# Optimization experiments

Measured on AMD Instinct MI355X. Metric: run time of the kernel, lower is better.

The kernel has to match this reference:

```python
import jax, jax.numpy as jnp
import numpy as np

B = 2          # graphs (images)
GRID = 13      # patches per spatial dim -> N = 169 patches per image
N = GRID * GRID
NN = B * N     # total nodes
C = 256        # hidden_dim / out_channels per head
H = 4          # attention heads
L = 3          # GAT layers
LRELU_SLOPE = 0.2
LN_EPS = 1e-5


def _dense_edges():
    # fully-connected directed graph (i != j) per image, as in create_graph
    idx = np.arange(N)
    src, dst = np.meshgrid(idx, idx, indexing='ij')
    mask = src != dst
    src, dst = src[mask], dst[mask]              # [N*(N-1)]
    offs = (np.arange(B) * N)[:, None]
    e_src = (src[None, :] + offs).reshape(-1)
    e_dst = (dst[None, :] + offs).reshape(-1)
    return e_src.astype(np.int32), e_dst.astype(np.int32)


def setup_inputs() -> dict:
    key = jax.random.key(0)
    ks = jax.random.split(key, 8)
    s = 0.05
    e_src, e_dst = _dense_edges()
    return {
        'x':   jax.random.normal(ks[0], (NN, C), jnp.float32),
        'Wl':  jax.random.normal(ks[1], (L, C, H * C), jnp.float32) * s,
        'bl':  jnp.zeros((L, H * C), jnp.float32),
        'Wr':  jax.random.normal(ks[2], (L, C, H * C), jnp.float32) * s,
        'br':  jnp.zeros((L, H * C), jnp.float32),
        'att': jax.random.normal(ks[3], (L, H, C), jnp.float32) * s,
        'bias': jnp.zeros((L, C), jnp.float32),
        'ln_g': jnp.ones((L, C), jnp.float32),
        'ln_b': jnp.zeros((L, C), jnp.float32),
        'W1':  jax.random.normal(ks[4], (L, C, 2 * C), jnp.float32) * s,
        'b1':  jnp.zeros((L, 2 * C), jnp.float32),
        'W2':  jax.random.normal(ks[5], (L, 2 * C, C), jnp.float32) * s,
        'b2':  jnp.zeros((L, C), jnp.float32),
        'edge_src': jnp.asarray(e_src),
        'edge_dst': jnp.asarray(e_dst),
        'batch_ids': jnp.repeat(jnp.arange(B, dtype=jnp.int32), N),
    }


def _gatv2(x, Wl, bl, Wr, br, att, bias, src, dst, n_nodes):
    # PyG GATv2Conv, concat=False (mean over heads)
    xl = (x @ Wl + bl).reshape(n_nodes, H, C)   # source transform
    xr = (x @ Wr + br).reshape(n_nodes, H, C)   # target transform
    e = jax.nn.leaky_relu(xl[src] + xr[dst], LRELU_SLOPE)     # [E,H,C]
    logits = jnp.einsum('ehc,hc->eh', e, att)                 # [E,H]
    m = jax.ops.segment_max(logits, dst, num_segments=n_nodes)
    a = jnp.exp(logits - m[dst])
    z = jax.ops.segment_sum(a, dst, num_segments=n_nodes)
    alpha = a / (z[dst] + 1e-16)                              # softmax per target
    msg = alpha[:, :, None] * xl[src]                         # [E,H,C]
    agg = jax.ops.segment_sum(msg, dst, num_segments=n_nodes) # [N,H,C]
    return agg.mean(axis=1) + bias


def _layernorm(x, g, b):
    mu = x.mean(-1, keepdims=True)
    var = jnp.mean((x - mu) ** 2, -1, keepdims=True)
    return (x - mu) * jax.lax.rsqrt(var + LN_EPS) * g + b


def reference(x, Wl, bl, Wr, br, att, bias, ln_g, ln_b, W1, b1, W2, b2,
              edge_src, edge_dst, batch_ids):
    n_nodes = x.shape[0]
    for l in range(L):
        residual = x
        h = _gatv2(x, Wl[l], bl[l], Wr[l], br[l], att[l], bias[l],
                   edge_src, edge_dst, n_nodes)
        h = _layernorm(h, ln_g[l], ln_b[l])
        mlp = jnp.maximum(h @ W1[l] + b1[l], 0.0) @ W2[l] + b2[l]
        x = residual + mlp
    # global mean pool per graph
    sums = jax.ops.segment_sum(x, batch_ids, num_segments=B)
    cnts = jax.ops.segment_sum(jnp.ones((n_nodes, 1), x.dtype), batch_ids,
                               num_segments=B)
    return sums / cnts
```

## Files before the change

kernel.cpp:

```cpp
#include <hip/hip_runtime.h>
#include <hip/hip_bf16.h>

typedef __hip_bfloat16 bf16;
typedef __attribute__((ext_vector_type(4))) float f32x4;
typedef __attribute__((ext_vector_type(8))) unsigned short u16x8;
typedef __attribute__((ext_vector_type(4))) unsigned short u16x4;
typedef __bf16 bf16x8 __attribute__((ext_vector_type(8)));

#define NNODES 169
#define NNTOT  338
#define CH     256
#define NH     4
#define NL     3
#define SPAD   176
#define LN_EPS 1e-5f

__device__ __forceinline__ float b2f(bf16 v) { return __bfloat162float(v); }
__device__ __forceinline__ float lrelu(float v) { return fmaxf(v, 0.2f * v); }
__device__ __forceinline__ float ldm(const void* p, size_t i, int isbf) {
    return isbf ? b2f(((const bf16*)p)[i]) : ((const float*)p)[i];
}
__device__ __forceinline__ int sniff_bf(const void* lng) {
    return ((((const unsigned*)lng)[0] & 0xFFFFu) == 0x3F80u) ? 1 : 0;
}
__device__ __forceinline__ unsigned short f2bf_rn(float f) {
    unsigned u = __float_as_uint(f);
    u += 0x7FFFu + ((u >> 16) & 1u);
    return (unsigned short)(u >> 16);
}
__device__ __forceinline__ float bfb2f(unsigned short h) {
    return __uint_as_float(((unsigned)h) << 16);
}

__global__ __launch_bounds__(256) void k_wprep(
    const void* __restrict__ Wl, const void* __restrict__ Wr,
    const void* __restrict__ W1, const void* __restrict__ W2,
    unsigned short* __restrict__ wlT, unsigned short* __restrict__ wrT,
    unsigned short* __restrict__ w1T, unsigned short* __restrict__ w2T,
    const void* __restrict__ lng)
{
    __shared__ unsigned short sH[64 * 72];
    __shared__ unsigned short sL[64 * 72];
    const int isbf = sniff_bf(lng);
    int t = blockIdx.x;
    const void* src; unsigned short* dst; int K, N;
    if (t < 384)      { K = 256; N = 1024; src = (t < 192) ? Wl : Wr;
                        dst = (t < 192) ? wlT : wrT; t = t % 192; }
    else if (t < 480) { K = 256; N = 512;  src = W1; dst = w1T; t -= 384; }
    else              { K = 512; N = 256;  src = W2; dst = w2T; t -= 480; }
    const int ntiles = N / 64;
    const int tpl = (K / 64) * ntiles;
    const int l = t / tpl; t %= tpl;
    const int k0 = (t / ntiles) * 64, n0 = (t % ntiles) * 64;
    const size_t loPlane = (size_t)NL * K * N;
    const int tid = threadIdx.x;

    const int kk = tid >> 2, q = tid & 3;
    if (isbf) {
        const bf16* srow = (const bf16*)src + ((size_t)l * K + k0 + kk) * N + n0;
        #pragma unroll
        for (int i = 0; i < 4; i++) {
            const int c = q * 4 + i * 16;
            const int2 w = *(const int2*)(srow + c);
            const unsigned short u0 = (unsigned short)(w.x & 0xFFFF);
            const unsigned short u1 = (unsigned short)(((unsigned)w.x) >> 16);
            const unsigned short u2 = (unsigned short)(w.y & 0xFFFF);
            const unsigned short u3 = (unsigned short)(((unsigned)w.y) >> 16);
            sH[kk * 72 + c + 0] = u0; sL[kk * 72 + c + 0] = 0;
            sH[kk * 72 + c + 1] = u1; sL[kk * 72 + c + 1] = 0;
            sH[kk * 72 + c + 2] = u2; sL[kk * 72 + c + 2] = 0;
            sH[kk * 72 + c + 3] = u3; sL[kk * 72 + c + 3] = 0;
        }
    } else {
        const float* srow = (const float*)src + ((size_t)l * K + k0 + kk) * N + n0;
        #pragma unroll
        for (int i = 0; i < 4; i++) {
            const int c = q * 4 + i * 16;
            const float4 v4 = *(const float4*)(srow + c);
            const float vv[4] = { v4.x, v4.y, v4.z, v4.w };
            #pragma unroll
            for (int j = 0; j < 4; j++) {
                const unsigned short h = f2bf_rn(vv[j]);
                sH[kk * 72 + c + j] = h;
                sL[kk * 72 + c + j] = f2bf_rn(vv[j] - bfb2f(h));
            }
        }
    }
    __syncthreads();
    for (int u = tid; u < 512; u += 256) {
        const int n = u >> 3, k8 = (u & 7) * 8;
        u16x8 hh, ll;
        #pragma unroll
        for (int j = 0; j < 8; j++) {
            hh[j] = sH[(k8 + j) * 72 + n];
            ll[j] = sL[(k8 + j) * 72 + n];
        }
        unsigned short* dh = dst + ((size_t)l * N + n0 + n) * K + k0 + k8;
        *(u16x8*)dh = hh;
        *(u16x8*)(dh + loPlane) = ll;
    }
}

__global__ __launch_bounds__(256) void k_gemm_mfma(
    const void* __restrict__ A, int a_raw, int K, int N,
    const unsigned short* __restrict__ wH0, const unsigned short* __restrict__ wL0,
    const unsigned short* __restrict__ wH1, const unsigned short* __restrict__ wL1,
    const void* __restrict__ bias0, const void* __restrict__ bias1, size_t oB,
    const void* __restrict__ res, int r_raw,
    float* __restrict__ out0, float* __restrict__ out1,
    float* __restrict__ xlT, int mode, const void* __restrict__ lng)
{
    __shared__ unsigned short sAh[32 * 40], sAl[32 * 40];
    __shared__ unsigned short sBh[64 * 40], sBl[64 * 40];
    const int isbf = sniff_bf(lng);
    const int z = blockIdx.z;
    const unsigned short* wH = z ? wH1 : wH0;
    const unsigned short* wL = z ? wL1 : wL0;
    const void* bias = z ? bias1 : bias0;
    float* out = z ? out1 : out0;
    const int a_bf = a_raw ? isbf : 0;
    const int tid = threadIdx.x;
    const int wave = tid >> 6, lane = tid & 63, l15 = lane & 15, g = lane >> 4;
    const int m0 = blockIdx.x * 32, n0 = blockIdx.y * 64;

    const int ar = tid >> 3, ak = (tid & 7) * 4;
    const int bn = tid >> 2, boct = tid & 3;

    f32x4 acc0 = {0.f, 0.f, 0.f, 0.f};
    f32x4 acc1 = {0.f, 0.f, 0.f, 0.f};
    const float* Af = (const float*)A;

    for (int k0 = 0; k0 < K; k0 += 32) {
        unsigned short h4[4] = {0, 0, 0, 0}, l4[4] = {0, 0, 0, 0};
        {
            const int grow = m0 + ar;
            if (grow < NNTOT) {
                const size_t ai = (size_t)grow * K + k0 + ak;
                if (a_bf) {
                    const int2 w = *(const int2*)((const bf16*)A + ai);
                    h4[0] = (unsigned short)(w.x & 0xFFFF);
                    h4[1] = (unsigned short)(((unsigned)w.x) >> 16);
                    h4[2] = (unsigned short)(w.y & 0xFFFF);
                    h4[3] = (unsigned short)(((unsigned)w.y) >> 16);
                } else {
                    const float4 t = *(const float4*)(Af + ai);
                    const float vv[4] = { t.x, t.y, t.z, t.w };
                    #pragma unroll
                    for (int j = 0; j < 4; j++) {
                        h4[j] = f2bf_rn(vv[j]);
                        l4[j] = f2bf_rn(vv[j] - bfb2f(h4[j]));
                    }
                }
            }
        }
        const size_t bi = (size_t)(n0 + bn) * K + k0 + boct * 8;
        const u16x8 bhv = *(const u16x8*)(wH + bi);
        const u16x8 blv = *(const u16x8*)(wL + bi);
        __syncthreads();
        {
            u16x4 ha, la;
            ha[0] = h4[0]; ha[1] = h4[1]; ha[2] = h4[2]; ha[3] = h4[3];
            la[0] = l4[0]; la[1] = l4[1]; la[2] = l4[2]; la[3] = l4[3];
            *(u16x4*)&sAh[ar * 40 + ak] = ha;
            *(u16x4*)&sAl[ar * 40 + ak] = la;
            *(u16x8*)&sBh[bn * 40 + boct * 8] = bhv;
            *(u16x8*)&sBl[bn * 40 + boct * 8] = blv;
        }
        __syncthreads();
        const bf16x8 a_h0 = *(const bf16x8*)&sAh[l15 * 40 + g * 8];
        const bf16x8 a_h1 = *(const bf16x8*)&sAh[(16 + l15) * 40 + g * 8];
        const bf16x8 a_l0 = *(const bf16x8*)&sAl[l15 * 40 + g * 8];
        const bf16x8 a_l1 = *(const bf16x8*)&sAl[(16 + l15) * 40 + g * 8];
        const bf16x8 b_h  = *(const bf16x8*)&sBh[(wave * 16 + l15) * 40 + g * 8];
        const bf16x8 b_l  = *(const bf16x8*)&sBl[(wave * 16 + l15) * 40 + g * 8];
        acc0 = __builtin_amdgcn_mfma_f32_16x16x32_bf16(a_h0, b_h, acc0, 0, 0, 0);
        acc1 = __builtin_amdgcn_mfma_f32_16x16x32_bf16(a_h1, b_h, acc1, 0, 0, 0);
        acc0 = __builtin_amdgcn_mfma_f32_16x16x32_bf16(a_l0, b_h, acc0, 0, 0, 0);
        acc1 = __builtin_amdgcn_mfma_f32_16x16x32_bf16(a_l1, b_h, acc1, 0, 0, 0);
        acc0 = __builtin_amdgcn_mfma_f32_16x16x32_bf16(a_h0, b_l, acc0, 0, 0, 0);
        acc1 = __builtin_amdgcn_mfma_f32_16x16x32_bf16(a_h1, b_l, acc1, 0, 0, 0);
    }

    const int col = n0 + wave * 16 + l15;
    const float bv = ldm(bias, oB + col, isbf);
    #pragma unroll
    for (int mi = 0; mi < 2; mi++) {
        const f32x4 a = mi ? acc1 : acc0;
        #pragma unroll
        for (int r = 0; r < 4; r++) {
            const int row = m0 + mi * 16 + g * 4 + r;
            if (row >= NNTOT) continue;
            float v = a[r] + bv;
            if (mode == 1) v = fmaxf(v, 0.f);
            if (mode == 2) v += ldm(res, (size_t)row * N + col, r_raw ? isbf : 0);
            out[(size_t)row * N + col] = v;
            if (mode == 0 && z == 0) {
                const int hh = col >> 8, cc = col & 255;
                const int gg = (row >= NNODES) ? 1 : 0;
                const int ss = row - gg * NNODES;
                xlT[((size_t)(gg * NH + hh) * CH + cc) * SPAD + ss] = v;
            }
        }
    }
}

__global__ __launch_bounds__(192) void k_logits_sm(
    const float* __restrict__ xlT, const float* __restrict__ xr,
    const void* __restrict__ att, size_t oA,
    float* __restrict__ alphaR, const void* __restrict__ lng)
{
    __shared__ float s_att[CH];
    __shared__ float s_xr[2 * CH];
    __shared__ float s_tile[32 * SPAD];
    __shared__ float s_log[2 * SPAD];
    const int isbf = sniff_bf(lng);
    const int g = blockIdx.z, h = blockIdx.y, d0 = blockIdx.x * 2;
    const int tid = threadIdx.x, lane = tid & 63, wv = tid >> 6;

    for (int idx = tid; idx < CH; idx += 192)
        s_att[idx] = ldm(att, oA + h * CH + idx, isbf);
    for (int idx = tid; idx < 2 * CH; idx += 192) {
        const int i = idx >> 8, c = idx & 255, d = d0 + i;
        s_xr[idx] = (d < NNODES)
            ? xr[(size_t)(g * NNODES + d) * (NH * CH) + h * CH + c] : 0.f;
    }

    float l0 = 0.f, l1 = 0.f;
    const int s = tid;
    const float4* src = (const float4*)(xlT + ((size_t)(g * NH + h) * CH) * SPAD);
    for (int ch = 0; ch < 8; ch++) {
        __syncthreads();
        #pragma unroll 2
        for (int i = tid; i < 32 * SPAD / 4; i += 192)
            ((float4*)s_tile)[i] = src[ch * (32 * SPAD / 4) + i];
        __syncthreads();
        if (s < NNODES) {
            const int cb = ch * 32;
            #pragma unroll
            for (int c = 0; c < 32; c++) {
                const float v = s_tile[c * SPAD + s];
                const float a = s_att[cb + c];
                l0 += a * lrelu(v + s_xr[cb + c]);
                l1 += a * lrelu(v + s_xr[CH + cb + c]);
            }
        }
    }
    if (s < NNODES) { s_log[s] = l0; s_log[SPAD + s] = l1; }
    __syncthreads();

    if (wv < 2) {
        const int d = d0 + wv;
        const float* row = s_log + wv * SPAD;
        const int s0 = lane, s1 = lane + 64, s2 = lane + 128;
        const float v0 = (s0 < NNODES && s0 != d) ? row[s0] : -1e30f;
        const float v1 = (s1 < NNODES && s1 != d) ? row[s1] : -1e30f;
        const float v2 = (s2 < NNODES && s2 != d) ? row[s2] : -1e30f;
        float mx = fmaxf(v0, fmaxf(v1, v2));
        mx = fmaxf(mx, __shfl_xor(mx, 32)); mx = fmaxf(mx, __shfl_xor(mx, 16));
        mx = fmaxf(mx, __shfl_xor(mx, 8));  mx = fmaxf(mx, __shfl_xor(mx, 4));
        mx = fmaxf(mx, __shfl_xor(mx, 2));  mx = fmaxf(mx, __shfl_xor(mx, 1));
        const float e0 = expf(v0 - mx), e1 = expf(v1 - mx), e2 = expf(v2 - mx);
        float zz = e0 + e1 + e2;
        zz += __shfl_xor(zz, 32); zz += __shfl_xor(zz, 16); zz += __shfl_xor(zz, 8);
        zz += __shfl_xor(zz, 4);  zz += __shfl_xor(zz, 2);  zz += __shfl_xor(zz, 1);
        const float sc = 0.25f / (zz + 1e-16f);
        if (d < NNODES) {
            float* arow = alphaR + ((size_t)(g * NH + h) * NNODES + d) * SPAD;
            if (s0 < NNODES) arow[s0] = e0 * sc;
            if (s1 < NNODES) arow[s1] = e1 * sc;
            if (s2 < NNODES) arow[s2] = e2 * sc;
        }
    }
}

__global__ __launch_bounds__(256) void k_agg(
    const float* __restrict__ alphaR, const float* __restrict__ xl,
    float* __restrict__ part)
{
    __shared__ float s_a[32 * 33];
    __shared__ float s_x[32 * 64];
    const int gh = blockIdx.z, g = gh >> 2, h = gh & 3;
    const int d0 = blockIdx.x * 32, c0 = blockIdx.y * 64;
    const int tid = threadIdx.x;
    const int dr = (tid >> 4) * 2, cq = (tid & 15) * 4;
    const int sr = tid >> 3, sc4 = (tid & 7) * 4;
    const int xc8 = (tid & 7) * 8;

    float acc[2][4] = {{0.f,0.f,0.f,0.f},{0.f,0.f,0.f,0.f}};

    for (int s0 = 0; s0 < NNODES; s0 += 32) {
        __syncthreads();
        {
            const int d = d0 + sr;
            const float* ap = alphaR + ((size_t)gh * NNODES + d) * SPAD + s0 + sc4;
            const int ok = (d < NNODES);
            s_a[sr * 33 + sc4 + 0] = (ok && s0 + sc4 + 0 < NNODES) ? ap[0] : 0.f;
            s_a[sr * 33 + sc4 + 1] = (ok && s0 + sc4 + 1 < NNODES) ? ap[1] : 0.f;
            s_a[sr * 33 + sc4 + 2] = (ok && s0 + sc4 + 2 < NNODES) ? ap[2] : 0.f;
            s_a[sr * 33 + sc4 + 3] = (ok && s0 + sc4 + 3 < NNODES) ? ap[3] : 0.f;
        }
        {
            const int sg = s0 + sr;
            if (sg < NNODES) {
                const float* xp = xl + (size_t)(g * NNODES + sg) * (NH * CH) + h * CH + c0 + xc8;
                *(float4*)&s_x[sr * 64 + xc8]     = *(const float4*)(xp);
                *(float4*)&s_x[sr * 64 + xc8 + 4] = *(const float4*)(xp + 4);
            } else {
                #pragma unroll
                for (int j = 0; j < 8; j++) s_x[sr * 64 + xc8 + j] = 0.f;
            }
        }
        __syncthreads();
        #pragma unroll
        for (int k = 0; k < 32; k++) {
            const float a0 = s_a[(dr + 0) * 33 + k];
            const float a1 = s_a[(dr + 1) * 33 + k];
            const float4 xv = *(const float4*)&s_x[k * 64 + cq];
            acc[0][0] += a0 * xv.x; acc[0][1] += a0 * xv.y;
            acc[0][2] += a0 * xv.z; acc[0][3] += a0 * xv.w;
            acc[1][0] += a1 * xv.x; acc[1][1] += a1 * xv.y;
            acc[1][2] += a1 * xv.z; acc[1][3] += a1 * xv.w;
        }
    }
    #pragma unroll
    for (int i = 0; i < 2; i++) {
        const int d = d0 + dr + i;
        if (d >= NNODES) continue;
        float4 v;
        v.x = acc[i][0]; v.y = acc[i][1]; v.z = acc[i][2]; v.w = acc[i][3];
        *(float4*)(part + ((size_t)h * NNTOT + g * NNODES + d) * CH + c0 + cq) = v;
    }
}

__global__ __launch_bounds__(256) void k_ln(
    const float* __restrict__ part,
    const void* __restrict__ bias, size_t oB,
    const void* __restrict__ ln_g, size_t oG,
    const void* __restrict__ ln_b, size_t oBt,
    float* __restrict__ h_out, const void* __restrict__ lng)
{
    __shared__ float s_red[8];
    const int isbf = sniff_bf(lng);
    const int node = blockIdx.x, c = threadIdx.x;
    const int lane = c & 63, wv = c >> 6;

    float vch = part[((size_t)0 * NNTOT + node) * CH + c]
              + part[((size_t)1 * NNTOT + node) * CH + c]
              + part[((size_t)2 * NNTOT + node) * CH + c]
              + part[((size_t)3 * NNTOT + node) * CH + c]
              + ldm(bias, oB + c, isbf);

    float s1 = vch, s2 = vch * vch;
    s1 += __shfl_xor(s1, 32); s2 += __shfl_xor(s2, 32);
    s1 += __shfl_xor(s1, 16); s2 += __shfl_xor(s2, 16);
    s1 += __shfl_xor(s1, 8);  s2 += __shfl_xor(s2, 8);
    s1 += __shfl_xor(s1, 4);  s2 += __shfl_xor(s2, 4);
    s1 += __shfl_xor(s1, 2);  s2 += __shfl_xor(s2, 2);
    s1 += __shfl_xor(s1, 1);  s2 += __shfl_xor(s2, 1);
    if (lane == 0) { s_red[wv] = s1; s_red[4 + wv] = s2; }
    __syncthreads();
    const float S1 = s_red[0] + s_red[1] + s_red[2] + s_red[3];
    const float S2 = s_red[4] + s_red[5] + s_red[6] + s_red[7];
    const float mu  = S1 * (1.f / CH);
    const float var = S2 * (1.f / CH) - mu * mu;
    const float o = (vch - mu) * rsqrtf(var + LN_EPS) * ldm(ln_g, oG + c, isbf)
                  + ldm(ln_b, oBt + c, isbf);
    h_out[(size_t)node * CH + c] = o;
}

__global__ __launch_bounds__(256) void k_pool(const float* __restrict__ x,
                                              void* __restrict__ out,
                                              const void* __restrict__ lng) {
    const int isbf = sniff_bf(lng);
    const int g = blockIdx.x, c = threadIdx.x;
    float s = 0.f;
    const float* p = x + (size_t)g * NNODES * CH + c;
    for (int n = 0; n < NNODES; n++) s += p[(size_t)n * CH];
    const float v = s * (1.f / NNODES);
    if (isbf) ((bf16*)out)[g * CH + c] = __float2bfloat16(v);
    else      ((float*)out)[g * CH + c] = v;
}

extern "C" void kernel_launch(void* const* d_in, const int* in_sizes, int n_in,
                              void* d_out, int out_size, void* d_ws, size_t ws_size,
                              hipStream_t stream)
{
    const void* x_in = d_in[0];
    const void* Wl   = d_in[1];
    const void* bl   = d_in[2];
    const void* Wr   = d_in[3];
    const void* br   = d_in[4];
    const void* att  = d_in[5];
    const void* bias = d_in[6];
    const void* lng  = d_in[7];
    const void* lnb  = d_in[8];
    const void* W1   = d_in[9];
    const void* b1   = d_in[10];
    const void* W2   = d_in[11];
    const void* b2   = d_in[12];

    float* ws     = (float*)d_ws;
    float* xl     = ws;
    float* xr     = xl + (size_t)NNTOT * NH * CH;
    float* xlT    = xr + (size_t)NNTOT * NH * CH;
    float* alphaR = xlT + (size_t)2 * NH * CH * SPAD;
    float* part   = alphaR + (size_t)2 * NH * NNODES * SPAD;
    float* h_ln   = part + (size_t)NH * NNTOT * CH;
    float* m1     = h_ln + (size_t)NNTOT * CH;
    float* xa     = m1 + (size_t)NNTOT * 2 * CH;
    float* xb     = xa + (size_t)NNTOT * CH;

    unsigned short* wbt = (unsigned short*)(xb + (size_t)NNTOT * CH);
    const size_t pLR = (size_t)NL * (NH * CH) * CH;
    const size_t pM  = (size_t)NL * (2 * CH) * CH;
    unsigned short* wlT = wbt;
    unsigned short* wrT = wlT + 2 * pLR;
    unsigned short* w1T = wrT + 2 * pLR;
    unsigned short* w2T = w1T + 2 * pM;
    const size_t lyLR = (size_t)(NH * CH) * CH;
    const size_t lyM  = (size_t)(2 * CH) * CH;

    const size_t sB  = NH * CH;
    const size_t sC  = CH;
    const size_t sB1 = 2 * CH;

    const void* x_l[3] = { x_in, xa, xb };
    float*      x_o[3] = { xa, xb, xa };

    k_wprep<<<dim3(576), 256, 0, stream>>>(Wl, Wr, W1, W2, wlT, wrT, w1T, w2T, lng);

    for (int l = 0; l < NL; l++) {
        const int israw = (l == 0);
        k_gemm_mfma<<<dim3(11, 16, 2), 256, 0, stream>>>(
            x_l[l], israw, CH, NH * CH,
            wlT + l * lyLR, wlT + pLR + l * lyLR,
            wrT + l * lyLR, wrT + pLR + l * lyLR,
            bl, br, (size_t)l * sB,
            nullptr, 0,
            xl, xr, xlT, 0, lng);
        k_logits_sm<<<dim3(85, NH, 2), 192, 0, stream>>>(
            xlT, xr, att, (size_t)l * sB, alphaR, lng);
        k_agg<<<dim3(6, 4, 8), 256, 0, stream>>>(alphaR, xl, part);
        k_ln<<<dim3(NNTOT), 256, 0, stream>>>(
            part, bias, (size_t)l * sC, lng, (size_t)l * sC, lnb, (size_t)l * sC,
            h_ln, lng);
        k_gemm_mfma<<<dim3(11, 8, 1), 256, 0, stream>>>(
            h_ln, 0, CH, 2 * CH,
            w1T + l * lyM, w1T + pM + l * lyM,
            w1T + l * lyM, w1T + pM + l * lyM,
            b1, b1, (size_t)l * sB1,
            nullptr, 0,
            m1, m1, nullptr, 1, lng);
        k_gemm_mfma<<<dim3(11, 4, 1), 256, 0, stream>>>(
            m1, 0, 2 * CH, CH,
            w2T + l * lyM, w2T + pM + l * lyM,
            w2T + l * lyM, w2T + pM + l * lyM,
            b2, b2, (size_t)l * sC,
            x_l[l], israw,
            x_o[l], x_o[l], nullptr, 2, lng);
    }

    k_pool<<<dim3(2), 256, 0, stream>>>(xa, d_out, lng);
}
```

Before: 327.7 us.

## Fuse attention softmax with aggregation and LayerNorm with first MLP GEMM

Merges the logits/softmax kernel with the alpha-weighted aggregation so alpha stays in shared memory and is never written to global memory. Each block now handles four targets instead of two, and the per-channel aggregation reads xl directly from global memory. It also fuses LayerNorm into the first MLP GEMM, normalising rows into split-bf16 shared tiles before the MFMA loop. This removes two kernel launches per layer and the h_ln and alphaR round trips. The trade-offs are that the aggregation now runs as scalar FMAs with strided global loads instead of a tiled kernel, and each LN block recomputes normalisation across all N tiles.

Measured after the change: 328.0 us. No clear change (+0.1%).

```diff
diff --git a/kernel.cpp b/kernel.cpp
--- a/kernel.cpp
+++ b/kernel.cpp
@@ -62,14 +62,12 @@
         for (int i = 0; i < 4; i++) {
             const int c = q * 4 + i * 16;
             const int2 w = *(const int2*)(srow + c);
-            const unsigned short u0 = (unsigned short)(w.x & 0xFFFF);
-            const unsigned short u1 = (unsigned short)(((unsigned)w.x) >> 16);
-            const unsigned short u2 = (unsigned short)(w.y & 0xFFFF);
-            const unsigned short u3 = (unsigned short)(((unsigned)w.y) >> 16);
-            sH[kk * 72 + c + 0] = u0; sL[kk * 72 + c + 0] = 0;
-            sH[kk * 72 + c + 1] = u1; sL[kk * 72 + c + 1] = 0;
-            sH[kk * 72 + c + 2] = u2; sL[kk * 72 + c + 2] = 0;
-            sH[kk * 72 + c + 3] = u3; sL[kk * 72 + c + 3] = 0;
+            sH[kk * 72 + c + 0] = (unsigned short)(w.x & 0xFFFF);
+            sH[kk * 72 + c + 1] = (unsigned short)(((unsigned)w.x) >> 16);
+            sH[kk * 72 + c + 2] = (unsigned short)(w.y & 0xFFFF);
+            sH[kk * 72 + c + 3] = (unsigned short)(((unsigned)w.y) >> 16);
+            sL[kk * 72 + c + 0] = 0; sL[kk * 72 + c + 1] = 0;
+            sL[kk * 72 + c + 2] = 0; sL[kk * 72 + c + 3] = 0;
         }
     } else {
         const float* srow = (const float*)src + ((size_t)l * K + k0 + kk) * N + n0;
@@ -191,7 +189,6 @@
             const int row = m0 + mi * 16 + g * 4 + r;
             if (row >= NNTOT) continue;
             float v = a[r] + bv;
-            if (mode == 1) v = fmaxf(v, 0.f);
             if (mode == 2) v += ldm(res, (size_t)row * N + col, r_raw ? isbf : 0);
             out[(size_t)row * N + col] = v;
             if (mode == 0 && z == 0) {
@@ -204,34 +201,33 @@
     }
 }
 
-__global__ __launch_bounds__(192) void k_logits_sm(
+__global__ __launch_bounds__(256) void k_attn(
     const float* __restrict__ xlT, const float* __restrict__ xr,
+    const float* __restrict__ xl,
     const void* __restrict__ att, size_t oA,
-    float* __restrict__ alphaR, const void* __restrict__ lng)
+    float* __restrict__ part, const void* __restrict__ lng)
 {
     __shared__ float s_att[CH];
-    __shared__ float s_xr[2 * CH];
+    __shared__ float s_xr[4 * CH];
     __shared__ float s_tile[32 * SPAD];
-    __shared__ float s_log[2 * SPAD];
+    __shared__ float s_log[4 * SPAD];
     const int isbf = sniff_bf(lng);
-    const int g = blockIdx.z, h = blockIdx.y, d0 = blockIdx.x * 2;
+    const int g = blockIdx.z, h = blockIdx.y, d0 = blockIdx.x * 4;
     const int tid = threadIdx.x, lane = tid & 63, wv = tid >> 6;
 
-    for (int idx = tid; idx < CH; idx += 192)
-        s_att[idx] = ldm(att, oA + h * CH + idx, isbf);
-    for (int idx = tid; idx < 2 * CH; idx += 192) {
+    s_att[tid] = ldm(att, oA + h * CH + tid, isbf);
+    for (int idx = tid; idx < 4 * CH; idx += 256) {
         const int i = idx >> 8, c = idx & 255, d = d0 + i;
         s_xr[idx] = (d < NNODES)
             ? xr[(size_t)(g * NNODES + d) * (NH * CH) + h * CH + c] : 0.f;
     }
 
-    float l0 = 0.f, l1 = 0.f;
+    float l0 = 0.f, l1 = 0.f, l2 = 0.f, l3 = 0.f;
     const int s = tid;
     const float4* src = (const float4*)(xlT + ((size_t)(g * NH + h) * CH) * SPAD);
     for (int ch = 0; ch < 8; ch++) {
         __syncthreads();
-        #pragma unroll 2
-        for (int i = tid; i < 32 * SPAD / 4; i += 192)
+        for (int i = tid; i < 32 * SPAD / 4; i += 256)
             ((float4*)s_tile)[i] = src[ch * (32 * SPAD / 4) + i];
         __syncthreads();
         if (s < NNODES) {
@@ -242,15 +238,19 @@
                 const float a = s_att[cb + c];
                 l0 += a * lrelu(v + s_xr[cb + c]);
                 l1 += a * lrelu(v + s_xr[CH + cb + c]);
+                l2 += a * lrelu(v + s_xr[2 * CH + cb + c]);
+                l3 += a * lrelu(v + s_xr[3 * CH + cb + c]);
             }
         }
     }
-    if (s < NNODES) { s_log[s] = l0; s_log[SPAD + s] = l1; }
+    if (s < NNODES) {
+        s_log[s] = l0; s_log[SPAD + s] = l1;
+        s_log[2 * SPAD + s] = l2; s_log[3 * SPAD + s] = l3;
+    }
     __syncthreads();
-
-    if (wv < 2) {
+    {
         const int d = d0 + wv;
-        const float* row = s_log + wv * SPAD;
+        float* row = s_log + wv * SPAD;
         const int s0 = lane, s1 = lane + 64, s2 = lane + 128;
         const float v0 = (s0 < NNODES && s0 != d) ? row[s0] : -1e30f;
         const float v1 = (s1 < NNODES && s1 != d) ? row[s1] : -1e30f;
@@ -264,108 +264,140 @@
         zz += __shfl_xor(zz, 32); zz += __shfl_xor(zz, 16); zz += __shfl_xor(zz, 8);
         zz += __shfl_xor(zz, 4);  zz += __shfl_xor(zz, 2);  zz += __shfl_xor(zz, 1);
         const float sc = 0.25f / (zz + 1e-16f);
-        if (d < NNODES) {
-            float* arow = alphaR + ((size_t)(g * NH + h) * NNODES + d) * SPAD;
-            if (s0 < NNODES) arow[s0] = e0 * sc;
-            if (s1 < NNODES) arow[s1] = e1 * sc;
-            if (s2 < NNODES) arow[s2] = e2 * sc;
-        }
-    }
-}
-
-__global__ __launch_bounds__(256) void k_agg(
-    const float* __restrict__ alphaR, const float* __restrict__ xl,
-    float* __restrict__ part)
-{
-    __shared__ float s_a[32 * 33];
-    __shared__ float s_x[32 * 64];
-    const int gh = blockIdx.z, g = gh >> 2, h = gh & 3;
-    const int d0 = blockIdx.x * 32, c0 = blockIdx.y * 64;
-    const int tid = threadIdx.x;
-    const int dr = (tid >> 4) * 2, cq = (tid & 15) * 4;
-    const int sr = tid >> 3, sc4 = (tid & 7) * 4;
-    const int xc8 = (tid & 7) * 8;
-
-    float acc[2][4] = {{0.f,0.f,0.f,0.f},{0.f,0.f,0.f,0.f}};
-
-    for (int s0 = 0; s0 < NNODES; s0 += 32) {
-        __syncthreads();
-        {
-            const int d = d0 + sr;
-            const float* ap = alphaR + ((size_t)gh * NNODES + d) * SPAD + s0 + sc4;
-            const int ok = (d < NNODES);
-            s_a[sr * 33 + sc4 + 0] = (ok && s0 + sc4 + 0 < NNODES) ? ap[0] : 0.f;
-            s_a[sr * 33 + sc4 + 1] = (ok && s0 + sc4 + 1 < NNODES) ? ap[1] : 0.f;
-            s_a[sr * 33 + sc4 + 2] = (ok && s0 + sc4 + 2 < NNODES) ? ap[2] : 0.f;
-            s_a[sr * 33 + sc4 + 3] = (ok && s0 + sc4 + 3 < NNODES) ? ap[3] : 0.f;
-        }
-        {
-            const int sg = s0 + sr;
-            if (sg < NNODES) {
-                const float* xp = xl + (size_t)(g * NNODES + sg) * (NH * CH) + h * CH + c0 + xc8;
-                *(float4*)&s_x[sr * 64 + xc8]     = *(const float4*)(xp);
-                *(float4*)&s_x[sr * 64 + xc8 + 4] = *(const float4*)(xp + 4);
-            } else {
-                #pragma unroll
-                for (int j = 0; j < 8; j++) s_x[sr * 64 + xc8 + j] = 0.f;
-            }
-        }
-        __syncthreads();
-        #pragma unroll
-        for (int k = 0; k < 32; k++) {
-            const float a0 = s_a[(dr + 0) * 33 + k];
-            const float a1 = s_a[(dr + 1) * 33 + k];
-            const float4 xv = *(const float4*)&s_x[k * 64 + cq];
-            acc[0][0] += a0 * xv.x; acc[0][1] += a0 * xv.y;
-            acc[0][2] += a0 * xv.z; acc[0][3] += a0 * xv.w;
-            acc[1][0] += a1 * xv.x; acc[1][1] += a1 * xv.y;
-            acc[1][2] += a1 * xv.z; acc[1][3] += a1 * xv.w;
-        }
-    }
+        row[s0] = (s0 < NNODES) ? e0 * sc : 0.f;
+        row[s1] = (s1 < NNODES) ? e1 * sc : 0.f;
+        if (s2 < SPAD) row[s2] = (s2 < NNODES) ? e2 * sc : 0.f;
+    }
+    __syncthreads();
+
+    const int c = tid;
+    float a0 = 0.f, a1 = 0.f, a2 = 0.f, a3 = 0.f;
+    const float* xbase = xl + (size_t)g * NNODES * (NH * CH) + h * CH + c;
+    for (int s4 = 0; s4 < 168; s4 += 4) {
+        const float4 q0 = *(const float4*)&s_log[s4];
+        const float4 q1 = *(const float4*)&s_log[SPAD + s4];
+        const float4 q2 = *(const float4*)&s_log[2 * SPAD + s4];
+        const float4 q3 = *(const float4*)&s_log[3 * SPAD + s4];
+        const float x0 = xbase[(size_t)(s4 + 0) * (NH * CH)];
+        const float x1 = xbase[(size_t)(s4 + 1) * (NH * CH)];
+        const float x2 = xbase[(size_t)(s4 + 2) * (NH * CH)];
+        const float x3 = xbase[(size_t)(s4 + 3) * (NH * CH)];
+        a0 += q0.x * x0 + q0.y * x1 + q0.z * x2 + q0.w * x3;
+        a1 += q1.x * x0 + q1.y * x1 + q1.z * x2 + q1.w * x3;
+        a2 += q2.x * x0 + q2.y * x1 + q2.z * x2 + q2.w * x3;
+        a3 += q3.x * x0 + q3.y * x1 + q3.z * x2 + q3.w * x3;
+    }
+    {
+        const float x0 = xbase[(size_t)168 * (NH * CH)];
+        a0 += s_log[168] * x0;            a1 += s_log[SPAD + 168] * x0;
+        a2 += s_log[2 * SPAD + 168] * x0; a3 += s_log[3 * SPAD + 168] * x0;
+    }
+    const float av[4] = { a0, a1, a2, a3 };
     #pragma unroll
-    for (int i = 0; i < 2; i++) {
-        const int d = d0 + dr + i;
-        if (d >= NNODES) continue;
-        float4 v;
-        v.x = acc[i][0]; v.y = acc[i][1]; v.z = acc[i][2]; v.w = acc[i][3];
-        *(float4*)(part + ((size_t)h * NNTOT + g * NNODES + d) * CH + c0 + cq) = v;
-    }
-}
-
-__global__ __launch_bounds__(256) void k_ln(
+    for (int i = 0; i < 4; i++) {
+        const int d = d0 + i;
+        if (d < NNODES)
+            part[((size_t)h * NNTOT + g * NNODES + d) * CH + c] = av[i];
+    }
+}
+
+__global__ __launch_bounds__(256) void k_lnmlp1(
     const float* __restrict__ part,
     const void* __restrict__ bias, size_t oB,
     const void* __restrict__ ln_g, size_t oG,
     const void* __restrict__ ln_b, size_t oBt,
-    float* __restrict__ h_out, const void* __restrict__ lng)
+    const unsigned short* __restrict__ wH, const unsigned short* __restrict__ wL,
+    const void* __restrict__ b1, size_t oB1,
+    float* __restrict__ m1, const void* __restrict__ lng)
 {
-    __shared__ float s_red[8];
+    __shared__ unsigned short sAh[32 * 264], sAl[32 * 264];
+    __shared__ unsigned short sBh[64 * 40], sBl[64 * 40];
+    __shared__ float sPar[3 * CH];
     const int isbf = sniff_bf(lng);
-    const int node = blockIdx.x, c = threadIdx.x;
-    const int lane = c & 63, wv = c >> 6;
-
-    float vch = part[((size_t)0 * NNTOT + node) * CH + c]
-              + part[((size_t)1 * NNTOT + node) * CH + c]
-              + part[((size_t)2 * NNTOT + node) * CH + c]
-              + part[((size_t)3 * NNTOT + node) * CH + c]
-              + ldm(bias, oB + c, isbf);
-
-    float s1 = vch, s2 = vch * vch;
-    s1 += __shfl_xor(s1, 32); s2 += __shfl_xor(s2, 32);
-    s1 += __shfl_xor(s1, 16); s2 += __shfl_xor(s2, 16);
-    s1 += __shfl_xor(s1, 8);  s2 += __shfl_xor(s2, 8);
-    s1 += __shfl_xor(s1, 4);  s2 += __shfl_xor(s2, 4);
-    s1 += __shfl_xor(s1, 2);  s2 += __shfl_xor(s2, 2);
-    s1 += __shfl_xor(s1, 1);  s2 += __shfl_xor(s2, 1);
-    if (lane == 0) { s_red[wv] = s1; s_red[4 + wv] = s2; }
+    const int tid = threadIdx.x;
+    const int wave = tid >> 6, lane = tid & 63, l15 = lane & 15, g = lane >> 4;
+    const int m0 = blockIdx.x * 32, n0 = blockIdx.y * 64;
+
+    sPar[tid]          = ldm(bias, oB + tid, isbf);
+    sPar[CH + tid]     = ldm(ln_g, oG + tid, isbf);
+    sPar[2 * CH + tid] = ldm(ln_b, oBt + tid, isbf);
     __syncthreads();
-    const float S1 = s_red[0] + s_red[1] + s_red[2] + s_red[3];
-    const float S2 = s_red[4] + s_red[5] + s_red[6] + s_red[7];
-    const float mu  = S1 * (1.f / CH);
-    const float var = S2 * (1.f / CH) - mu * mu;
-    const float o = (vch - mu) * rsqrtf(var + LN_EPS) * ldm(ln_g, oG + c, isbf)
-                  + ldm(ln_b, oBt + c, isbf);
-    h_out[(size_t)node * CH + c] = o;
+
+    const int c4 = lane * 4;
+    #pragma unroll
+    for (int rr = 0; rr < 8; rr++) {
+        const int r = wave + rr * 4;
+        const int gr = m0 + r;
+        u16x4 hq = {0, 0, 0, 0}, lq = {0, 0, 0, 0};
+        if (gr < NNTOT) {
+            const float4 p0 = *(const float4*)(part + ((size_t)0 * NNTOT + gr) * CH + c4);
+            const float4 p1 = *(const float4*)(part + ((size_t)1 * NNTOT + gr) * CH + c4);
+            const float4 p2 = *(const float4*)(part + ((size_t)2 * NNTOT + gr) * CH + c4);
+            const float4 p3 = *(const float4*)(part + ((size_t)3 * NNTOT + gr) * CH + c4);
+            float v[4] = { p0.x + p1.x + p2.x + p3.x + sPar[c4 + 0],
+                           p0.y + p1.y + p2.y + p3.y + sPar[c4 + 1],
+                           p0.z + p1.z + p2.z + p3.z + sPar[c4 + 2],
+                           p0.w + p1.w + p2.w + p3.w + sPar[c4 + 3] };
+            float s1 = v[0] + v[1] + v[2] + v[3];
+            float s2 = v[0]*v[0] + v[1]*v[1] + v[2]*v[2] + v[3]*v[3];
+            s1 += __shfl_xor(s1, 32); s2 += __shfl_xor(s2, 32);
+            s1 += __shfl_xor(s1, 16); s2 += __shfl_xor(s2, 16);
+            s1 += __shfl_xor(s1, 8);  s2 += __shfl_xor(s2, 8);
+            s1 += __shfl_xor(s1, 4);  s2 += __shfl_xor(s2, 4);
+            s1 += __shfl_xor(s1, 2);  s2 += __shfl_xor(s2, 2);
+            s1 += __shfl_xor(s1, 1);  s2 += __shfl_xor(s2, 1);
+            const float mu  = s1 * (1.f / CH);
+            const float var = s2 * (1.f / CH) - mu * mu;
+            const float rs  = rsqrtf(var + LN_EPS);
+            #pragma unroll
+            for (int j = 0; j < 4; j++) {
+                const float o = (v[j] - mu) * rs * sPar[CH + c4 + j] + sPar[2 * CH + c4 + j];
+                const unsigned short hh = f2bf_rn(o);
+                hq[j] = hh;
+                lq[j] = f2bf_rn(o - bfb2f(hh));
+            }
+        }
+        *(u16x4*)&sAh[r * 264 + c4] = hq;
+        *(u16x4*)&sAl[r * 264 + c4] = lq;
+    }
+
+    const int bn = tid >> 2, boct = tid & 3;
+    f32x4 acc0 = {0.f, 0.f, 0.f, 0.f};
+    f32x4 acc1 = {0.f, 0.f, 0.f, 0.f};
+    for (int k0 = 0; k0 < CH; k0 += 32) {
+        const size_t bi = (size_t)(n0 + bn) * CH + k0 + boct * 8;
+        const u16x8 bhv = *(const u16x8*)(wH + bi);
+        const u16x8 blv = *(const u16x8*)(wL + bi);
+        __syncthreads();
+        *(u16x8*)&sBh[bn * 40 + boct * 8] = bhv;
+        *(u16x8*)&sBl[bn * 40 + boct * 8] = blv;
+        __syncthreads();
+        const bf16x8 a_h0 = *(const bf16x8*)&sAh[l15 * 264 + k0 + g * 8];
+        const bf16x8 a_h1 = *(const bf16x8*)&sAh[(16 + l15) * 264 + k0 + g * 8];
+        const bf16x8 a_l0 = *(const bf16x8*)&sAl[l15 * 264 + k0 + g * 8];
+        const bf16x8 a_l1 = *(const bf16x8*)&sAl[(16 + l15) * 264 + k0 + g * 8];
+        const bf16x8 b_h  = *(const bf16x8*)&sBh[(wave * 16 + l15) * 40 + g * 8];
+        const bf16x8 b_l  = *(const bf16x8*)&sBl[(wave * 16 + l15) * 40 + g * 8];
+        acc0 = __builtin_amdgcn_mfma_f32_16x16x32_bf16(a_h0, b_h, acc0, 0, 0, 0);
+        acc1 = __builtin_amdgcn_mfma_f32_16x16x32_bf16(a_h1, b_h, acc1, 0, 0, 0);
+        acc0 = __builtin_amdgcn_mfma_f32_16x16x32_bf16(a_l0, b_h, acc0, 0, 0, 0);
+        acc1 = __builtin_amdgcn_mfma_f32_16x16x32_bf16(a_l1, b_h, acc1, 0, 0, 0);
+        acc0 = __builtin_amdgcn_mfma_f32_16x16x32_bf16(a_h0, b_l, acc0, 0, 0, 0);
+        acc1 = __builtin_amdgcn_mfma_f32_16x16x32_bf16(a_h1, b_l, acc1, 0, 0, 0);
+    }
+
+    const int col = n0 + wave * 16 + l15;
+    const float bv = ldm(b1, oB1 + col, isbf);
+    #pragma unroll
+    for (int mi = 0; mi < 2; mi++) {
+        const f32x4 a = mi ? acc1 : acc0;
+        #pragma unroll
+        for (int r = 0; r < 4; r++) {
+            const int row = m0 + mi * 16 + g * 4 + r;
+            if (row >= NNTOT) continue;
+            m1[(size_t)row * (2 * CH) + col] = fmaxf(a[r] + bv, 0.f);
+        }
+    }
 }
 
 __global__ __launch_bounds__(256) void k_pool(const float* __restrict__ x,
@@ -403,10 +435,8 @@
     float* xl     = ws;
     float* xr     = xl + (size_t)NNTOT * NH * CH;
     float* xlT    = xr + (size_t)NNTOT * NH * CH;
-    float* alphaR = xlT + (size_t)2 * NH * CH * SPAD;
-    float* part   = alphaR + (size_t)2 * NH * NNODES * SPAD;
-    float* h_ln   = part + (size_t)NH * NNTOT * CH;
-    float* m1     = h_ln + (size_t)NNTOT * CH;
+    float* part   = xlT + (size_t)2 * NH * CH * SPAD;
+    float* m1     = part + (size_t)NH * NNTOT * CH;
     float* xa     = m1 + (size_t)NNTOT * 2 * CH;
     float* xb     = xa + (size_t)NNTOT * CH;
 
@@ -420,10 +450,6 @@
     const size_t lyLR = (size_t)(NH * CH) * CH;
     const size_t lyM  = (size_t)(2 * CH) * CH;
 
-    const size_t sB  = NH * CH;
-    const size_t sC  = CH;
-    const size_t sB1 = 2 * CH;
-
     const void* x_l[3] = { x_in, xa, xb };
     float*      x_o[3] = { xa, xb, xa };
 
@@ -435,27 +461,20 @@
             x_l[l], israw, CH, NH * CH,
             wlT + l * lyLR, wlT + pLR + l * lyLR,
             wrT + l * lyLR, wrT + pLR + l * lyLR,
-            bl, br, (size_t)l * sB,
+            bl, br, (size_t)l * (NH * CH),
             nullptr, 0,
             xl, xr, xlT, 0, lng);
-        k_logits_sm<<<dim3(85, NH, 2), 192, 0, stream>>>(
-            xlT, xr, att, (size_t)l * sB, alphaR, lng);
-        k_agg<<<dim3(6, 4, 8), 256, 0, stream>>>(alphaR, xl, part);
-        k_ln<<<dim3(NNTOT), 256, 0, stream>>>(
-            part, bias, (size_t)l * sC, lng, (size_t)l * sC, lnb, (size_t)l * sC,
-            h_ln, lng);
-        k_gemm_mfma<<<dim3(11, 8, 1), 256, 0, stream>>>(
-            h_ln, 0, CH, 2 * CH,
+        k_attn<<<dim3(43, NH, 2), 256, 0, stream>>>(
+            xlT, xr, xl, att, (size_t)l * (NH * CH), part, lng);
+        k_lnmlp1<<<dim3(11, 8), 256, 0, stream>>>(
+            part, bias, (size_t)l * CH, lng, (size_t)l * CH, lnb, (size_t)l * CH,
             w1T + l * lyM, w1T + pM + l * lyM,
-            w1T + l * lyM, w1T + pM + l * lyM,
-            b1, b1, (size_t)l * sB1,
-            nullptr, 0,
-            m1, m1, nullptr, 1, lng);
+            b1, (size_t)l * (2 * CH), m1, lng);
         k_gemm_mfma<<<dim3(11, 4, 1), 256, 0, stream>>>(
             m1, 0, 2 * CH, CH,
             w2T + l * lyM, w2T + pM + l * lyM,
             w2T + l * lyM, w2T + pM + l * lyM,
-            b2, b2, (size_t)l * sC,
+            b2, b2, (size_t)l * CH,
             x_l[l], israw,
             x_o[l], x_o[l], nullptr, 2, lng);
     }
```
